# Performance work log

Measured on AMD Instinct MI355X. Metric: run time of the kernel, lower is better.

## Reference

```python
import jax, jax.numpy as jnp
import numpy as np

P = 128          # feat_dim
K_CLS = 1000     # num_classes
TAU = 0.1
ORDER = P // 2 - 1   # Bessel order p/2 - 1 = 63


def _log_bessel_miller(kappa):
    """log I_{P/2-1}(kappa) via Miller backward recurrence (M = P), kappa: (N,).
    Carried trial values are rescaled when they overflow float32; the final
    ratio I0_exact * I_target/I0_trial is scale-invariant so math is unchanged."""
    safe_k = jnp.maximum(kappa, 1e-10)
    nus = jnp.arange(P, -1, -1, dtype=jnp.float32)  # nu = M..0

    def step(carry, nu):
        I_curr, I_next, I_tgt, I_zero = carry
        I_prev = 2.0 * nu / safe_k * I_curr + I_next
        I_tgt = jnp.where(nu == ORDER + 1.0, I_curr, I_tgt)
        I_zero = jnp.where(nu == 1.0, I_curr, I_zero)
        scale = jnp.where(I_prev > 1e30, 1e-30, 1.0)
        return (I_prev * scale, I_curr * scale, I_tgt * scale, I_zero * scale), None

    init = (jnp.ones_like(kappa), jnp.zeros_like(kappa),
            jnp.zeros_like(kappa), jnp.zeros_like(kappa))
    (_, _, I_tgt, I_zero), _ = jax.lax.scan(step, init, nus)
    i0_exact = jax.scipy.special.i0(jnp.minimum(kappa, 700.0))
    bessel = i0_exact / jnp.maximum(I_zero, 1e-30) * I_tgt
    return jnp.log(jnp.maximum(bessel, 1e-30))


def _log_Cp(kappa):
    kappa = jnp.maximum(kappa, 1e-8)
    val = (P / 2.0 - 1.0) * jnp.log(kappa) \
        - (P / 2.0) * np.log(2.0 * np.pi) - _log_bessel_miller(kappa)
    return jnp.clip(val, -500.0, 500.0)


def setup_inputs() -> dict:
    key = jax.random.key(0)
    k1, k2, k3, k4 = jax.random.split(key, 4)
    B = 8192
    features = jax.random.normal(k1, (B, P), dtype=jnp.float32)
    labels = jax.random.randint(k2, (B,), 0, K_CLS)
    class_prior = jax.random.uniform(k3, (K_CLS,), jnp.float32, 0.01, 1.0)
    class_prior = class_prior / jnp.sum(class_prior)
    # previous-epoch class means on the unit ball, norm ~0.5 -> realistic kappa
    z_bar = jax.random.normal(k4, (K_CLS, P), dtype=jnp.float32) * (0.5 / np.sqrt(P))
    return {"features": features, "labels": labels,
            "class_prior": class_prior, "z_bar": z_bar}


def reference(features, labels, class_prior, z_bar):
    # --- normalize features (F.normalize with eps=1e-8, then nan_to_num) ---
    feats = features.astype(jnp.float32)
    nrm = jnp.maximum(jnp.linalg.norm(feats, axis=1, keepdims=True), 1e-8)
    feats = jnp.nan_to_num(feats / nrm)

    # --- estimate_vmf_params ---
    zb = jnp.nan_to_num(z_bar)
    R = jnp.clip(jnp.linalg.norm(zb, axis=1), 0.0, 1.0 - 1e-6)          # (K,)
    mu = jnp.where((R > 1e-8)[:, None], zb / jnp.maximum(R, 1e-8)[:, None], 0.0)
    mu = mu / jnp.maximum(jnp.linalg.norm(mu, axis=1, keepdims=True), 1e-8)
    R2 = R * R
    kappa = jnp.clip(R * (P - R2) / jnp.maximum(1.0 - R2, 1e-8), 1e-3, 50.0)

    log_Cp_kappa = _log_Cp(kappa)                                        # (K,)

    # --- kappa_tilde_ij = || kappa_j mu_j + z_i/tau ||, expanded norm to
    #     avoid the (B,K,P) intermediate; same math. ---
    km = kappa[:, None] * mu                                             # (K,P)
    z_tau = feats / TAU                                                  # (B,P)
    sq = jnp.sum(km * km, axis=1)                                        # (K,)
    zsq = jnp.sum(z_tau * z_tau, axis=1)                                 # (B,)
    cross = 2.0 * (z_tau @ km.T)                                         # (B,K)
    kt2 = jnp.maximum(sq[None, :] + cross + zsq[:, None], 0.0)
    kappa_tilde = jnp.clip(jnp.sqrt(kt2), 1e-4, 50.0)                    # (B,K)

    log_Cp_kt = _log_Cp(kappa_tilde.reshape(-1)).reshape(kappa_tilde.shape)

    log_pi = jnp.log(jnp.maximum(class_prior, 1e-8))
    log_ratio = jnp.clip(log_pi[None, :] + log_Cp_kt - log_Cp_kappa[None, :],
                         -500.0, 500.0)                                  # (B,K)

    B = feats.shape[0]
    log_num = log_ratio[jnp.arange(B), labels]
    log_den = jax.nn.logsumexp(log_ratio, axis=1)
    loss = jnp.mean(-log_num + log_den)
    return jnp.nan_to_num(loss, nan=0.0, posinf=10.0, neginf=-10.0)
```

## Files before the change

kernel.cpp:

```cpp
#include <hip/hip_runtime.h>
#include <math.h>

#define K_CLS 1000
#define P_DIM 128
#define MAGICU 0x5EEDBA5Eu

typedef __attribute__((ext_vector_type(8))) short short8v;
typedef __attribute__((ext_vector_type(4))) unsigned int uint4v;
typedef __attribute__((ext_vector_type(4))) float f32x4;

__device__ __forceinline__ float fexp2(float x){ return __builtin_amdgcn_exp2f(x); }
__device__ __forceinline__ float flog2(float x){ return __builtin_amdgcn_logf(x); }
__device__ __forceinline__ float fsqrt_(float x){ return __builtin_amdgcn_sqrtf(x); }
__device__ __forceinline__ float frcp_(float x){ return __builtin_amdgcn_rcpf(x); }

__device__ __forceinline__ float gpoly(float u) {
    float w = fsqrt_(fmaf(u, 2.51952633e-4f, 1.0f));
    float v = w - 1.0f;
    return v * fmaf(v, fmaf(v, 3.456560f, -11.647408f), -44.726690f);
}

__device__ __forceinline__ unsigned short f2bf(float f) {
    unsigned int u = __float_as_uint(f);
    unsigned int r = (u + 0x7FFFu + ((u >> 16) & 1u)) >> 16;
    return (unsigned short)r;
}
__device__ __forceinline__ unsigned pk2(float lo, float hi) {
    return __builtin_amdgcn_perm(__float_as_uint(hi), __float_as_uint(lo), 0x07060302u);
}
__device__ __forceinline__ short8v pk8(float4 a, float4 b) {
    uint4v u;
    u[0] = pk2(a.x, a.y); u[1] = pk2(a.z, a.w);
    u[2] = pk2(b.x, b.y); u[3] = pk2(b.z, b.w);
    return __builtin_bit_cast(short8v, u);
}

__global__ __launch_bounds__(256) void prep_kernel(
    const float* __restrict__ z_bar, const float* __restrict__ prior,
    short8v* __restrict__ kmF, float2* __restrict__ cls2)
{
    __shared__ float kmS[16][132];
    const int bid = blockIdx.x, t = threadIdx.x, w = t >> 6, lane = t & 63;

    #pragma unroll
    for (int rr = 0; rr < 4; ++rr) {
        const int kc = w * 4 + rr;
        const int k = bid * 16 + kc;
        if (k < K_CLS) {
            float zb0 = z_bar[k * P_DIM + lane];
            float zb1 = z_bar[k * P_DIM + 64 + lane];
            float ss = fmaf(zb0, zb0, zb1 * zb1);
            #pragma unroll
            for (int off = 32; off >= 1; off >>= 1) ss += __shfl_xor(ss, off, 64);
            float nzb = sqrtf(ss);
            float R   = fminf(nzb, 1.0f - 1e-6f);
            float R2  = R * R;
            float kap = fminf(fmaxf(R * (128.0f - R2) * frcp_(fmaxf(1.0f - R2, 1e-8f)),
                                    1e-3f), 50.0f);
            bool ok   = R > 1e-8f;
            float fscl = ok ? kap * frcp_(nzb) : 0.0f;
            float sq   = ok ? kap * kap : 0.0f;
            kmS[kc][lane] = zb0 * fscl; kmS[kc][64 + lane] = zb1 * fscl;
            if (lane == 0) {
                float cc2 = flog2(fmaxf(prior[k], 1e-8f)) - gpoly(sq);
                cls2[k] = make_float2(cc2, sq);
            }
        } else {
            kmS[kc][lane] = 0.0f; kmS[kc][64 + lane] = 0.0f;
            if (lane == 0) cls2[k] = make_float2(-1.0e5f, 0.0f);
        }
    }
    __syncthreads();
    {
        const int ks = w;
        const float* src = &kmS[lane & 15][ks * 32 + (lane >> 4) * 8];
        float4 a = *(const float4*)src;
        float4 b = *(const float4*)(src + 4);
        short8v fr;
        fr[0] = (short)f2bf(a.x); fr[1] = (short)f2bf(a.y);
        fr[2] = (short)f2bf(a.z); fr[3] = (short)f2bf(a.w);
        fr[4] = (short)f2bf(b.x); fr[5] = (short)f2bf(b.y);
        fr[6] = (short)f2bf(b.z); fr[7] = (short)f2bf(b.w);
        kmF[(bid * 4 + ks) * 64 + lane] = fr;
    }
}

__global__ __launch_bounds__(512, 4) void main_kernel(
    const float* __restrict__ feats, const int* __restrict__ labels,
    const short8v* __restrict__ kmF, const float2* __restrict__ cls2,
    float* __restrict__ out, long long* __restrict__ part,
    unsigned* __restrict__ ptagB, int B)
{
    __shared__ float zS[16][132];
    __shared__ float zsqS[16];
    __shared__ int   labS[16];
    __shared__ float sW[8][16];
    __shared__ float nW[8][16];
    __shared__ long long redq[8];

    const int t = threadIdx.x, lane = t & 63, w = t >> 6, bid = blockIdx.x;
    const int g = lane >> 4, c16 = lane & 15;
    const int rowbase = bid * 16;

    #pragma unroll
    for (int rr = 0; rr < 2; ++rr) {
        const int r = w * 2 + rr;
        const float* f = feats + (size_t)(rowbase + r) * P_DIM;
        float2 v = *(const float2*)(f + lane * 2);
        float ss = fmaf(v.x, v.x, v.y * v.y);
        #pragma unroll
        for (int off = 32; off >= 1; off >>= 1) ss += __shfl_xor(ss, off, 64);
        float rn = frcp_(fmaxf(fsqrt_(ss), 1e-8f)) * 10.0f;
        float z0 = v.x * rn;
        float z1 = v.y * rn;
        float zq = fmaf(z0, z0, z1 * z1);
        #pragma unroll
        for (int off = 32; off >= 1; off >>= 1) zq += __shfl_xor(zq, off, 64);
        zS[r][2 * lane] = z0; zS[r][2 * lane + 1] = z1;
        if (lane == 0) { zsqS[r] = zq; labS[r] = labels[rowbase + r]; }
    }
    __syncthreads();

    short8v aF[4];
    #pragma unroll
    for (int ks = 0; ks < 4; ++ks) {
        const float* src = &zS[c16][ks * 32 + g * 8];
        aF[ks] = pk8(*(const float4*)src, *(const float4*)(src + 4));
    }

    float zsqv[4], sAc[4], nAc[4]; int labv[4];
    #pragma unroll
    for (int r = 0; r < 4; ++r) {
        zsqv[r] = zsqS[g * 4 + r];
        labv[r] = labS[g * 4 + r];
        sAc[r] = 0.0f; nAc[r] = -1e30f;
    }

    #pragma unroll 2
    for (int tt = 0; tt < 8; ++tt) {
        const int cb = w * 8 + tt;
        short8v b0 = kmF[(cb * 4 + 0) * 64 + lane];
        short8v b1 = kmF[(cb * 4 + 1) * 64 + lane];
        short8v b2 = kmF[(cb * 4 + 2) * 64 + lane];
        short8v b3 = kmF[(cb * 4 + 3) * 64 + lane];
        const int c = (cb << 4) + c16;
        const float2 cs = cls2[c];
        f32x4 acc = {0.0f, 0.0f, 0.0f, 0.0f};
        acc = __builtin_amdgcn_mfma_f32_16x16x32_bf16(aF[0], b0, acc, 0, 0, 0);
        acc = __builtin_amdgcn_mfma_f32_16x16x32_bf16(aF[1], b1, acc, 0, 0, 0);
        acc = __builtin_amdgcn_mfma_f32_16x16x32_bf16(aF[2], b2, acc, 0, 0, 0);
        acc = __builtin_amdgcn_mfma_f32_16x16x32_bf16(aF[3], b3, acc, 0, 0, 0);
        #pragma unroll
        for (int r = 0; r < 4; ++r) {
            float u = fmaf(2.0f, acc[r], cs.y + zsqv[r]);
            u = fminf(fmaxf(u, 1e-8f), 2500.0f);
            float lr2 = cs.x + gpoly(u);
            nAc[r] = (c == labv[r]) ? lr2 : nAc[r];
            sAc[r] += fexp2(lr2);
        }
    }

    #pragma unroll
    for (int off = 1; off < 16; off <<= 1) {
        #pragma unroll
        for (int r = 0; r < 4; ++r) {
            sAc[r] += __shfl_xor(sAc[r], off, 64);
            nAc[r] = fmaxf(nAc[r], __shfl_xor(nAc[r], off, 64));
        }
    }
    if (c16 == 0) {
        #pragma unroll
        for (int r = 0; r < 4; ++r) {
            sW[w][g * 4 + r] = sAc[r];
            nW[w][g * 4 + r] = nAc[r];
        }
    }
    __syncthreads();

    long long q = 0;
    if (t < 16) {
        float S = 0.0f, NUM = -1e30f;
        #pragma unroll
        for (int w2 = 0; w2 < 8; ++w2) { S += sW[w2][t]; NUM = fmaxf(NUM, nW[w2][t]); }
        float rl = 0.6931471805599453f * (flog2(S) - NUM);
        q = (long long)rintf(rl * 1073741824.0f);
    }
    if (w == 0) {
        #pragma unroll
        for (int off = 1; off < 16; off <<= 1) q += __shfl_xor(q, off, 64);
        if (lane == 0) {
            __hip_atomic_store(&part[bid], q, __ATOMIC_RELAXED,
                               __HIP_MEMORY_SCOPE_AGENT);
            asm volatile("s_waitcnt vmcnt(0)" ::: "memory");
            __hip_atomic_store(&ptagB[bid], MAGICU, __ATOMIC_RELAXED,
                               __HIP_MEMORY_SCOPE_AGENT);
        }
    }

    if (bid == 0) {
        while (__hip_atomic_load(&ptagB[t], __ATOMIC_RELAXED,
                                 __HIP_MEMORY_SCOPE_AGENT) != MAGICU)
            __builtin_amdgcn_s_sleep(2);
        __syncthreads();
        if (t == 0)
            (void)__hip_atomic_load(&ptagB[0], __ATOMIC_ACQUIRE, __HIP_MEMORY_SCOPE_AGENT);
        __syncthreads();
        long long q2 = __hip_atomic_load(&part[t], __ATOMIC_RELAXED,
                                         __HIP_MEMORY_SCOPE_AGENT);
        #pragma unroll
        for (int off = 1; off < 64; off <<= 1) q2 += __shfl_xor(q2, off, 64);
        if (lane == 0) redq[w] = q2;
        __syncthreads();
        if (t == 0) {
            long long tot = 0;
            #pragma unroll
            for (int w2 = 0; w2 < 8; ++w2) tot += redq[w2];
            float loss = (float)(((double)tot) / 1073741824.0 / (double)B);
            if (isnan(loss)) loss = 0.0f;
            else if (isinf(loss)) loss = loss > 0.0f ? 10.0f : -10.0f;
            out[0] = loss;
        }
    }
}

extern "C" void kernel_launch(void* const* d_in, const int* in_sizes, int n_in,
                              void* d_out, int out_size, void* d_ws, size_t ws_size,
                              hipStream_t stream) {
    const float* feats  = (const float*)d_in[0];
    const int*   labels = (const int*)d_in[1];
    const float* prior  = (const float*)d_in[2];
    const float* z_bar  = (const float*)d_in[3];
    float* out = (float*)d_out;
    int B = in_sizes[1];

    char* ws = (char*)d_ws;
    short8v*   kmF   = (short8v*)ws;
    float2*    cls2  = (float2*)(ws + 262144);
    long long* part  = (long long*)(ws + 262144 + 8192);
    unsigned*  ptagB = (unsigned*)(ws + 262144 + 8192 + 4096);

    prep_kernel<<<64, 256, 0, stream>>>(z_bar, prior, kmF, cls2);
    main_kernel<<<B / 16, 512, 0, stream>>>(feats, labels, kmF, cls2, out,
                                            part, ptagB, B);
}
```

Baseline: 20.89 us.

## Fuse prep kernel into main kernel with flag-based inter-block sync

Merges the class-parameter prep kernel into the main kernel. The first 64 blocks compute the bf16 kappa*mu fragments and per-class constants, then publish a per-block magic tag with a release store. Every block normalizes its features first and then spin-waits on all 64 tags before starting the MFMA loop. This removes one kernel launch and the gap between launches, but it relies on the first 64 blocks being co-resident or scheduled early, and it adds spin-wait latency.

```diff
diff --git a/kernel.cpp b/kernel.cpp
--- a/kernel.cpp
+++ b/kernel.cpp
@@ -35,62 +35,14 @@
     return __builtin_bit_cast(short8v, u);
 }
 
-__global__ __launch_bounds__(256) void prep_kernel(
-    const float* __restrict__ z_bar, const float* __restrict__ prior,
-    short8v* __restrict__ kmF, float2* __restrict__ cls2)
+__global__ __launch_bounds__(512, 4) void fused_kernel(
+    const float* __restrict__ feats, const int* __restrict__ labels,
+    const float* __restrict__ prior, const float* __restrict__ z_bar,
+    float* __restrict__ out, short8v* __restrict__ kmF, float2* __restrict__ cls2,
+    unsigned* __restrict__ ptagP, long long* __restrict__ part,
+    unsigned* __restrict__ ptagB, int B)
 {
     __shared__ float kmS[16][132];
-    const int bid = blockIdx.x, t = threadIdx.x, w = t >> 6, lane = t & 63;
-
-    #pragma unroll
-    for (int rr = 0; rr < 4; ++rr) {
-        const int kc = w * 4 + rr;
-        const int k = bid * 16 + kc;
-        if (k < K_CLS) {
-            float zb0 = z_bar[k * P_DIM + lane];
-            float zb1 = z_bar[k * P_DIM + 64 + lane];
-            float ss = fmaf(zb0, zb0, zb1 * zb1);
-            #pragma unroll
-            for (int off = 32; off >= 1; off >>= 1) ss += __shfl_xor(ss, off, 64);
-            float nzb = sqrtf(ss);
-            float R   = fminf(nzb, 1.0f - 1e-6f);
-            float R2  = R * R;
-            float kap = fminf(fmaxf(R * (128.0f - R2) * frcp_(fmaxf(1.0f - R2, 1e-8f)),
-                                    1e-3f), 50.0f);
-            bool ok   = R > 1e-8f;
-            float fscl = ok ? kap * frcp_(nzb) : 0.0f;
-            float sq   = ok ? kap * kap : 0.0f;
-            kmS[kc][lane] = zb0 * fscl; kmS[kc][64 + lane] = zb1 * fscl;
-            if (lane == 0) {
-                float cc2 = flog2(fmaxf(prior[k], 1e-8f)) - gpoly(sq);
-                cls2[k] = make_float2(cc2, sq);
-            }
-        } else {
-            kmS[kc][lane] = 0.0f; kmS[kc][64 + lane] = 0.0f;
-            if (lane == 0) cls2[k] = make_float2(-1.0e5f, 0.0f);
-        }
-    }
-    __syncthreads();
-    {
-        const int ks = w;
-        const float* src = &kmS[lane & 15][ks * 32 + (lane >> 4) * 8];
-        float4 a = *(const float4*)src;
-        float4 b = *(const float4*)(src + 4);
-        short8v fr;
-        fr[0] = (short)f2bf(a.x); fr[1] = (short)f2bf(a.y);
-        fr[2] = (short)f2bf(a.z); fr[3] = (short)f2bf(a.w);
-        fr[4] = (short)f2bf(b.x); fr[5] = (short)f2bf(b.y);
-        fr[6] = (short)f2bf(b.z); fr[7] = (short)f2bf(b.w);
-        kmF[(bid * 4 + ks) * 64 + lane] = fr;
-    }
-}
-
-__global__ __launch_bounds__(512, 4) void main_kernel(
-    const float* __restrict__ feats, const int* __restrict__ labels,
-    const short8v* __restrict__ kmF, const float2* __restrict__ cls2,
-    float* __restrict__ out, long long* __restrict__ part,
-    unsigned* __restrict__ ptagB, int B)
-{
     __shared__ float zS[16][132];
     __shared__ float zsqS[16];
     __shared__ int   labS[16];
@@ -102,6 +54,54 @@
     const int g = lane >> 4, c16 = lane & 15;
     const int rowbase = bid * 16;
 
+    if (bid < 64) {
+        #pragma unroll
+        for (int rr = 0; rr < 2; ++rr) {
+            const int kc = w * 2 + rr;
+            const int k = bid * 16 + kc;
+            if (k < K_CLS) {
+                float zb0 = z_bar[k * P_DIM + lane];
+                float zb1 = z_bar[k * P_DIM + 64 + lane];
+                float ss = fmaf(zb0, zb0, zb1 * zb1);
+                #pragma unroll
+                for (int off = 32; off >= 1; off >>= 1) ss += __shfl_xor(ss, off, 64);
+                float nzb = sqrtf(ss);
+                float R   = fminf(nzb, 1.0f - 1e-6f);
+                float R2  = R * R;
+                float kap = fminf(fmaxf(R * (128.0f - R2) * frcp_(fmaxf(1.0f - R2, 1e-8f)),
+                                        1e-3f), 50.0f);
+                bool ok   = R > 1e-8f;
+                float fscl = ok ? kap * frcp_(nzb) : 0.0f;
+                float sq   = ok ? kap * kap : 0.0f;
+                kmS[kc][lane] = zb0 * fscl; kmS[kc][64 + lane] = zb1 * fscl;
+                if (lane == 0) {
+                    float cc2 = flog2(fmaxf(prior[k], 1e-8f)) - gpoly(sq);
+                    cls2[k] = make_float2(cc2, sq);
+                }
+            } else {
+                kmS[kc][lane] = 0.0f; kmS[kc][64 + lane] = 0.0f;
+                if (lane == 0) cls2[k] = make_float2(-1.0e5f, 0.0f);
+            }
+        }
+        __syncthreads();
+        if (w < 4) {
+            const int ks = w;
+            const float* src = &kmS[lane & 15][ks * 32 + (lane >> 4) * 8];
+            float4 a = *(const float4*)src;
+            float4 b = *(const float4*)(src + 4);
+            short8v fr;
+            fr[0] = (short)f2bf(a.x); fr[1] = (short)f2bf(a.y);
+            fr[2] = (short)f2bf(a.z); fr[3] = (short)f2bf(a.w);
+            fr[4] = (short)f2bf(b.x); fr[5] = (short)f2bf(b.y);
+            fr[6] = (short)f2bf(b.z); fr[7] = (short)f2bf(b.w);
+            kmF[(bid * 4 + ks) * 64 + lane] = fr;
+        }
+        __syncthreads();
+        if (t == 0)
+            __hip_atomic_store(&ptagP[bid], MAGICU, __ATOMIC_RELEASE,
+                               __HIP_MEMORY_SCOPE_AGENT);
+    }
+
     #pragma unroll
     for (int rr = 0; rr < 2; ++rr) {
         const int r = w * 2 + rr;
@@ -135,6 +135,19 @@
         labv[r] = labS[g * 4 + r];
         sAc[r] = 0.0f; nAc[r] = -1e30f;
     }
+
+    if (w == 0) {
+        for (;;) {
+            unsigned v = __hip_atomic_load(&ptagP[lane], __ATOMIC_RELAXED,
+                                           __HIP_MEMORY_SCOPE_AGENT);
+            if (__all(v == MAGICU)) break;
+            __builtin_amdgcn_s_sleep(2);
+        }
+    }
+    __syncthreads();
+    if (t == 0)
+        (void)__hip_atomic_load(&ptagP[0], __ATOMIC_ACQUIRE, __HIP_MEMORY_SCOPE_AGENT);
+    __syncthreads();
 
     #pragma unroll 2
     for (int tt = 0; tt < 8; ++tt) {
@@ -236,10 +249,10 @@
     char* ws = (char*)d_ws;
     short8v*   kmF   = (short8v*)ws;
     float2*    cls2  = (float2*)(ws + 262144);
-    long long* part  = (long long*)(ws + 262144 + 8192);
-    unsigned*  ptagB = (unsigned*)(ws + 262144 + 8192 + 4096);
-
-    prep_kernel<<<64, 256, 0, stream>>>(z_bar, prior, kmF, cls2);
-    main_kernel<<<B / 16, 512, 0, stream>>>(feats, labels, kmF, cls2, out,
-                                            part, ptagB, B);
-}
+    unsigned*  ptagP = (unsigned*)(ws + 262144 + 8192);
+    long long* part  = (long long*)(ws + 262144 + 8192 + 256);
+    unsigned*  ptagB = (unsigned*)(ws + 262144 + 8192 + 256 + 4096);
+
+    fused_kernel<<<B / 16, 512, 0, stream>>>(feats, labels, prior, z_bar, out,
+                                             kmF, cls2, ptagP, part, ptagB, B);
+}
```

Result: slower. 22.73 us (+8.8%).

## Split class dimension across two blocks per row tile with cross-block merge

Applied to the files above, without the earlier changes.

Each 16-row tile is now processed by two blocks, each covering half of the class blocks, which doubles the grid and halves per-block MFMA/epilogue work. The second half publishes its partial sum and max-label values per row to global memory with a flag, and the first half spins on that flag before finishing the per-row log-sum and the global reduction. Launch bounds are raised to 8 blocks per CU and the inner loop interleaves the B-fragment loads with the MFMAs. This trades more redundant feature normalization, extra spin-wait synchronization and a second cross-block handshake for more parallelism and occupancy.

```diff
diff --git a/kernel.cpp b/kernel.cpp
--- a/kernel.cpp
+++ b/kernel.cpp
@@ -85,10 +85,11 @@
     }
 }
 
-__global__ __launch_bounds__(512, 4) void main_kernel(
+__global__ __launch_bounds__(512, 8) void main_kernel(
     const float* __restrict__ feats, const int* __restrict__ labels,
     const short8v* __restrict__ kmF, const float2* __restrict__ cls2,
-    float* __restrict__ out, long long* __restrict__ part,
+    float* __restrict__ out, unsigned long long* __restrict__ Ph,
+    unsigned* __restrict__ ptagH, long long* __restrict__ part,
     unsigned* __restrict__ ptagB, int B)
 {
     __shared__ float zS[16][132];
@@ -99,8 +100,9 @@
     __shared__ long long redq[8];
 
     const int t = threadIdx.x, lane = t & 63, w = t >> 6, bid = blockIdx.x;
+    const int rowTile = bid >> 1, half = bid & 1;
     const int g = lane >> 4, c16 = lane & 15;
-    const int rowbase = bid * 16;
+    const int rowbase = rowTile * 16;
 
     #pragma unroll
     for (int rr = 0; rr < 2; ++rr) {
@@ -136,20 +138,21 @@
         sAc[r] = 0.0f; nAc[r] = -1e30f;
     }
 
-    #pragma unroll 2
-    for (int tt = 0; tt < 8; ++tt) {
-        const int cb = w * 8 + tt;
-        short8v b0 = kmF[(cb * 4 + 0) * 64 + lane];
-        short8v b1 = kmF[(cb * 4 + 1) * 64 + lane];
-        short8v b2 = kmF[(cb * 4 + 2) * 64 + lane];
-        short8v b3 = kmF[(cb * 4 + 3) * 64 + lane];
+    #pragma unroll 1
+    for (int tt = 0; tt < 4; ++tt) {
+        const int cb = half * 32 + w * 4 + tt;
+        const short8v* kb = kmF + cb * 256;
+        short8v b0 = kb[lane];
+        short8v b1 = kb[64 + lane];
+        f32x4 acc = {0.0f, 0.0f, 0.0f, 0.0f};
+        acc = __builtin_amdgcn_mfma_f32_16x16x32_bf16(aF[0], b0, acc, 0, 0, 0);
+        short8v b2 = kb[128 + lane];
+        acc = __builtin_amdgcn_mfma_f32_16x16x32_bf16(aF[1], b1, acc, 0, 0, 0);
+        short8v b3 = kb[192 + lane];
+        acc = __builtin_amdgcn_mfma_f32_16x16x32_bf16(aF[2], b2, acc, 0, 0, 0);
+        acc = __builtin_amdgcn_mfma_f32_16x16x32_bf16(aF[3], b3, acc, 0, 0, 0);
         const int c = (cb << 4) + c16;
         const float2 cs = cls2[c];
-        f32x4 acc = {0.0f, 0.0f, 0.0f, 0.0f};
-        acc = __builtin_amdgcn_mfma_f32_16x16x32_bf16(aF[0], b0, acc, 0, 0, 0);
-        acc = __builtin_amdgcn_mfma_f32_16x16x32_bf16(aF[1], b1, acc, 0, 0, 0);
-        acc = __builtin_amdgcn_mfma_f32_16x16x32_bf16(aF[2], b2, acc, 0, 0, 0);
-        acc = __builtin_amdgcn_mfma_f32_16x16x32_bf16(aF[3], b3, acc, 0, 0, 0);
         #pragma unroll
         for (int r = 0; r < 4; ++r) {
             float u = fmaf(2.0f, acc[r], cs.y + zsqv[r]);
@@ -177,11 +180,44 @@
     }
     __syncthreads();
 
+    float Sk = 0.0f, Nk = -1e30f;
+    if (t < 16) {
+        #pragma unroll
+        for (int w2 = 0; w2 < 8; ++w2) { Sk += sW[w2][t]; Nk = fmaxf(Nk, nW[w2][t]); }
+    }
+
+    if (half == 1) {
+        if (t < 16) {
+            unsigned long long pk = (unsigned long long)__float_as_uint(Sk)
+                                  | ((unsigned long long)__float_as_uint(Nk) << 32);
+            __hip_atomic_store(&Ph[rowbase + t], pk, __ATOMIC_RELAXED,
+                               __HIP_MEMORY_SCOPE_AGENT);
+        }
+        if (t == 0) {
+            asm volatile("s_waitcnt vmcnt(0)" ::: "memory");
+            __hip_atomic_store(&ptagH[rowTile], MAGICU, __ATOMIC_RELAXED,
+                               __HIP_MEMORY_SCOPE_AGENT);
+        }
+        return;
+    }
+
+    if (t == 0) {
+        while (__hip_atomic_load(&ptagH[rowTile], __ATOMIC_RELAXED,
+                                 __HIP_MEMORY_SCOPE_AGENT) != MAGICU)
+            __builtin_amdgcn_s_sleep(2);
+        (void)__hip_atomic_load(&ptagH[rowTile], __ATOMIC_ACQUIRE,
+                                __HIP_MEMORY_SCOPE_AGENT);
+    }
+    __syncthreads();
+
     long long q = 0;
     if (t < 16) {
-        float S = 0.0f, NUM = -1e30f;
-        #pragma unroll
-        for (int w2 = 0; w2 < 8; ++w2) { S += sW[w2][t]; NUM = fmaxf(NUM, nW[w2][t]); }
+        unsigned long long pk = __hip_atomic_load(&Ph[rowbase + t], __ATOMIC_RELAXED,
+                                                  __HIP_MEMORY_SCOPE_AGENT);
+        float S1 = __uint_as_float((unsigned)pk);
+        float N1 = __uint_as_float((unsigned)(pk >> 32));
+        float S  = Sk + S1;
+        float NUM = fmaxf(Nk, N1);
         float rl = 0.6931471805599453f * (flog2(S) - NUM);
         q = (long long)rintf(rl * 1073741824.0f);
     }
@@ -189,10 +225,10 @@
         #pragma unroll
         for (int off = 1; off < 16; off <<= 1) q += __shfl_xor(q, off, 64);
         if (lane == 0) {
-            __hip_atomic_store(&part[bid], q, __ATOMIC_RELAXED,
+            __hip_atomic_store(&part[rowTile], q, __ATOMIC_RELAXED,
                                __HIP_MEMORY_SCOPE_AGENT);
             asm volatile("s_waitcnt vmcnt(0)" ::: "memory");
-            __hip_atomic_store(&ptagB[bid], MAGICU, __ATOMIC_RELAXED,
+            __hip_atomic_store(&ptagB[rowTile], MAGICU, __ATOMIC_RELAXED,
                                __HIP_MEMORY_SCOPE_AGENT);
         }
     }
@@ -234,12 +270,14 @@
     int B = in_sizes[1];
 
     char* ws = (char*)d_ws;
-    short8v*   kmF   = (short8v*)ws;
-    float2*    cls2  = (float2*)(ws + 262144);
-    long long* part  = (long long*)(ws + 262144 + 8192);
-    unsigned*  ptagB = (unsigned*)(ws + 262144 + 8192 + 4096);
+    short8v*            kmF   = (short8v*)ws;
+    float2*             cls2  = (float2*)(ws + 262144);
+    unsigned long long* Ph    = (unsigned long long*)(ws + 262144 + 8192);
+    long long*          part  = (long long*)(ws + 262144 + 8192 + 65536);
+    unsigned*           ptagH = (unsigned*)(ws + 262144 + 8192 + 65536 + 4096);
+    unsigned*           ptagB = (unsigned*)(ws + 262144 + 8192 + 65536 + 4096 + 2048);
 
     prep_kernel<<<64, 256, 0, stream>>>(z_bar, prior, kmF, cls2);
-    main_kernel<<<B / 16, 512, 0, stream>>>(feats, labels, kmF, cls2, out,
-                                            part, ptagB, B);
-}
+    main_kernel<<<(B / 16) * 2, 512, 0, stream>>>(feats, labels, kmF, cls2, out,
+                                                  Ph, ptagH, part, ptagB, B);
+}
```

After: 27.48 us. +31.6%, slower.

## Prefetch class tiles with register double buffering and split MFMA accumulators

Applied to the files above, without the earlier changes.

Moves the first class-mean fragment loads and all per-class constants ahead of the feature normalization, so their global latency overlaps the row prologue. The class loop is fully unrolled and double-buffered in registers, loading the next tile's fragments while the current tile's MFMAs run. The four dependent MFMAs are split into two independent accumulator chains to shorten the dependency chain. The cost is higher VGPR pressure, which under launch bounds of 512 threads and 4 blocks could cause spills or lower occupancy.

```diff
diff --git a/kernel.cpp b/kernel.cpp
--- a/kernel.cpp
+++ b/kernel.cpp
@@ -101,6 +101,14 @@
     const int t = threadIdx.x, lane = t & 63, w = t >> 6, bid = blockIdx.x;
     const int g = lane >> 4, c16 = lane & 15;
     const int rowbase = bid * 16;
+    const int cb0 = w * 8;
+
+    short8v bA[4], bB[4];
+    #pragma unroll
+    for (int j = 0; j < 4; ++j) bA[j] = kmF[(cb0 * 4 + j) * 64 + lane];
+    float2 csv[8];
+    #pragma unroll
+    for (int tt = 0; tt < 8; ++tt) csv[tt] = cls2[((cb0 + tt) << 4) + c16];
 
     #pragma unroll
     for (int rr = 0; rr < 2; ++rr) {
@@ -136,23 +144,26 @@
         sAc[r] = 0.0f; nAc[r] = -1e30f;
     }
 
-    #pragma unroll 2
+    #pragma unroll
     for (int tt = 0; tt < 8; ++tt) {
-        const int cb = w * 8 + tt;
-        short8v b0 = kmF[(cb * 4 + 0) * 64 + lane];
-        short8v b1 = kmF[(cb * 4 + 1) * 64 + lane];
-        short8v b2 = kmF[(cb * 4 + 2) * 64 + lane];
-        short8v b3 = kmF[(cb * 4 + 3) * 64 + lane];
-        const int c = (cb << 4) + c16;
-        const float2 cs = cls2[c];
-        f32x4 acc = {0.0f, 0.0f, 0.0f, 0.0f};
-        acc = __builtin_amdgcn_mfma_f32_16x16x32_bf16(aF[0], b0, acc, 0, 0, 0);
-        acc = __builtin_amdgcn_mfma_f32_16x16x32_bf16(aF[1], b1, acc, 0, 0, 0);
-        acc = __builtin_amdgcn_mfma_f32_16x16x32_bf16(aF[2], b2, acc, 0, 0, 0);
-        acc = __builtin_amdgcn_mfma_f32_16x16x32_bf16(aF[3], b3, acc, 0, 0, 0);
+        short8v* cur = (tt & 1) ? bB : bA;
+        short8v* nxt = (tt & 1) ? bA : bB;
+        if (tt < 7) {
+            const int cbn = cb0 + tt + 1;
+            #pragma unroll
+            for (int j = 0; j < 4; ++j) nxt[j] = kmF[(cbn * 4 + j) * 64 + lane];
+        }
+        f32x4 z4 = {0.0f, 0.0f, 0.0f, 0.0f};
+        f32x4 acc0 = __builtin_amdgcn_mfma_f32_16x16x32_bf16(aF[0], cur[0], z4, 0, 0, 0);
+        f32x4 acc1 = __builtin_amdgcn_mfma_f32_16x16x32_bf16(aF[1], cur[1], z4, 0, 0, 0);
+        acc0 = __builtin_amdgcn_mfma_f32_16x16x32_bf16(aF[2], cur[2], acc0, 0, 0, 0);
+        acc1 = __builtin_amdgcn_mfma_f32_16x16x32_bf16(aF[3], cur[3], acc1, 0, 0, 0);
+
+        const int c = ((cb0 + tt) << 4) + c16;
+        const float2 cs = csv[tt];
         #pragma unroll
         for (int r = 0; r < 4; ++r) {
-            float u = fmaf(2.0f, acc[r], cs.y + zsqv[r]);
+            float u = fmaf(2.0f, acc0[r], fmaf(2.0f, acc1[r], cs.y + zsqv[r]));
             u = fminf(fmaxf(u, 1e-8f), 2500.0f);
             float lr2 = cs.x + gpoly(u);
             nAc[r] = (c == labv[r]) ? lr2 : nAc[r];
```

Result: slower. 21.48 us (+2.8%).
